# Performance work log

Measured on AMD Instinct MI355X. Metric: run time of the kernel, lower is better.

Reference implementation:

```python
import jax, jax.numpy as jnp
import numpy as np

HEADS = 8
DIM_HEAD = 64
DIM = 512
EPS = 1e-5


def setup_inputs() -> dict:
    key = jax.random.key(0)
    ks = jax.random.split(key, 4)
    b, n = 4, 2048
    inner = HEADS * DIM_HEAD
    x = jax.random.normal(ks[0], (b, n, DIM), dtype=jnp.float32)
    pose_bias = jax.random.normal(ks[1], (b, n), dtype=jnp.float32)
    ln_gamma = jnp.ones((DIM,), dtype=jnp.float32)
    ln_beta = jnp.zeros((DIM,), dtype=jnp.float32)
    w_qkv = jax.random.normal(ks[2], (DIM, 3 * inner), dtype=jnp.float32) * (DIM ** -0.5)
    w_out = jax.random.normal(ks[3], (inner, DIM), dtype=jnp.float32) * (inner ** -0.5)
    beta = jnp.float32(0.5)
    return {"x": x, "pose_bias": pose_bias, "ln_gamma": ln_gamma,
            "ln_beta": ln_beta, "w_qkv": w_qkv, "w_out": w_out, "beta": beta}


def reference(x, pose_bias, ln_gamma, ln_beta, w_qkv, w_out, beta):
    b, n, d = x.shape
    h, dh = HEADS, DIM_HEAD
    scale = dh ** -0.5
    # LayerNorm (biased variance, eps=1e-5, affine)
    mu = jnp.mean(x, axis=-1, keepdims=True)
    var = jnp.mean(jnp.square(x - mu), axis=-1, keepdims=True)
    xn = (x - mu) * jax.lax.rsqrt(var + EPS) * ln_gamma + ln_beta
    # fused QKV projection (no bias)
    qkv = xn @ w_qkv                                  # [b, n, 3*h*dh]
    q, k, v = jnp.split(qkv, 3, axis=-1)
    def to_heads(t):
        return t.reshape(b, n, h, dh).transpose(0, 2, 1, 3)  # [b, h, n, dh]
    q, k, v = to_heads(q), to_heads(k), to_heads(v)
    dots = jnp.einsum('bhnd,bhmd->bhnm', q, k) * scale  # [b, h, n, n]
    # additive pose bias: beta * (bias_i + bias_j), broadcast over heads
    pose_attn = beta * (pose_bias[:, None, :, None] + pose_bias[:, None, None, :])
    dots = dots + pose_attn
    attn = jax.nn.softmax(dots, axis=-1)
    out = jnp.einsum('bhnm,bhmd->bhnd', attn, v)       # [b, h, n, dh]
    out = out.transpose(0, 2, 1, 3).reshape(b, n, h * dh)
    return out @ w_out
```

## Files before the change

kernel.cpp:

```cpp
#include <hip/hip_runtime.h>

#define NH    8
#define DH    64
#define DIMD  512
#define NCTX  2048
#define NB    4
#define NROWS (NB * NCTX)
#define QKVN  (3 * DIMD)

typedef __attribute__((ext_vector_type(8))) short bf16x8;
typedef __attribute__((ext_vector_type(4))) float f32x4;

#define INV_LN2 1.44269504f
#define SCLOG   (0.125f * INV_LN2)

__device__ __forceinline__ unsigned short f2bits(float f) {
  unsigned u = __float_as_uint(f);
  u += 0x7fffu + ((u >> 16) & 1u);
  return (unsigned short)(u >> 16);
}
__device__ __forceinline__ float bits2f(unsigned short u) {
  return __uint_as_float(((unsigned)u) << 16);
}

__device__ __forceinline__ void gll16(const void* g, void* l) {
  __builtin_amdgcn_global_load_lds(
      (const __attribute__((address_space(1))) unsigned int*)g,
      (__attribute__((address_space(3))) unsigned int*)l, 16, 0, 0);
}
__device__ __forceinline__ void gll4(const void* g, void* l) {
  __builtin_amdgcn_global_load_lds(
      (const __attribute__((address_space(1))) unsigned int*)g,
      (__attribute__((address_space(3))) unsigned int*)l, 4, 0, 0);
}

__global__ __launch_bounds__(256) void lntc_kernel(
    const float* __restrict__ x,
    const float* __restrict__ gamma,
    const float* __restrict__ beta,
    unsigned short* __restrict__ xn,
    const float* __restrict__ in0, unsigned short* __restrict__ out0,
    const float* __restrict__ in1, unsigned short* __restrict__ out1) {
  __shared__ float T[64][65];
  if (blockIdx.x < 2048) {
    const int wid  = threadIdx.x >> 6;
    const int lane = threadIdx.x & 63;
    const int row  = blockIdx.x * 4 + wid;
    const float* xr = x + (size_t)row * DIMD + lane * 8;
    float v[8];
    const float4 a = *reinterpret_cast<const float4*>(xr);
    const float4 b = *reinterpret_cast<const float4*>(xr + 4);
    v[0] = a.x; v[1] = a.y; v[2] = a.z; v[3] = a.w;
    v[4] = b.x; v[5] = b.y; v[6] = b.z; v[7] = b.w;
    float s = 0.f;
#pragma unroll
    for (int i = 0; i < 8; ++i) s += v[i];
#pragma unroll
    for (int off = 32; off; off >>= 1) s += __shfl_down(s, off);
    s = __shfl(s, 0);
    const float mu = s * (1.f / DIMD);
    float ss = 0.f;
#pragma unroll
    for (int i = 0; i < 8; ++i) { float d = v[i] - mu; ss += d * d; }
#pragma unroll
    for (int off = 32; off; off >>= 1) ss += __shfl_down(ss, off);
    ss = __shfl(ss, 0);
    const float inv = rsqrtf(ss * (1.f / DIMD) + 1e-5f);
    const float4 g0 = *reinterpret_cast<const float4*>(gamma + lane * 8);
    const float4 g1 = *reinterpret_cast<const float4*>(gamma + lane * 8 + 4);
    const float4 b0 = *reinterpret_cast<const float4*>(beta + lane * 8);
    const float4 b1 = *reinterpret_cast<const float4*>(beta + lane * 8 + 4);
    float g[8] = {g0.x, g0.y, g0.z, g0.w, g1.x, g1.y, g1.z, g1.w};
    float be[8] = {b0.x, b0.y, b0.z, b0.w, b1.x, b1.y, b1.z, b1.w};
    bf16x8 o;
#pragma unroll
    for (int i = 0; i < 8; ++i)
      o[i] = (short)f2bits((v[i] - mu) * inv * g[i] + be[i]);
    *reinterpret_cast<bf16x8*>(xn + (size_t)row * DIMD + lane * 8) = o;
  } else {
    const int t = blockIdx.x - 2048;
    const int bx = t % 24, rest = t / 24;
    const int by = rest % 8, z = rest / 8;
    const int C = z ? DIMD : QKVN;
    if (z && bx >= DIMD / 64) return;
    const float* in = z ? in1 : in0;
    unsigned short* out = z ? out1 : out0;
    const int r0 = by * 64, c0 = bx * 64;
    const int ty = threadIdx.x >> 4, tx = threadIdx.x & 15;
#pragma unroll
    for (int i = 0; i < 4; ++i) {
      const int r = ty + i * 16;
      const float4 v = *reinterpret_cast<const float4*>(
          in + (size_t)(r0 + r) * C + c0 + tx * 4);
      T[r][tx * 4 + 0] = v.x; T[r][tx * 4 + 1] = v.y;
      T[r][tx * 4 + 2] = v.z; T[r][tx * 4 + 3] = v.w;
    }
    __syncthreads();
#pragma unroll
    for (int i = 0; i < 4; ++i) {
      const int c = ty + i * 16;
      ushort4 o;
      o.x = f2bits(T[tx * 4 + 0][c]); o.y = f2bits(T[tx * 4 + 1][c]);
      o.z = f2bits(T[tx * 4 + 2][c]); o.w = f2bits(T[tx * 4 + 3][c]);
      *reinterpret_cast<ushort4*>(out + (size_t)(c0 + c) * DIMD + r0 + tx * 4) = o;
    }
  }
}

__global__ __launch_bounds__(256) void vtrans_kernel(
    const unsigned short* __restrict__ qkv,
    const float* __restrict__ pb,
    const float* __restrict__ betap,
    unsigned short* __restrict__ cexp,
    unsigned short* __restrict__ vt) {
  __shared__ unsigned short T[64][68];
  const int jt = blockIdx.x, hi = blockIdx.y, bi = blockIdx.z;
  const int ty = threadIdx.x >> 4, tx = threadIdx.x & 15;
  const int j0 = jt * 64;
#pragma unroll
  for (int i = 0; i < 4; ++i) {
    const int j = ty + i * 16;
    const ushort4 v = *reinterpret_cast<const ushort4*>(
        qkv + (size_t)(bi * NCTX + j0 + j) * QKVN + 2 * DIMD + hi * DH + tx * 4);
    T[j][tx * 4 + 0] = v.x; T[j][tx * 4 + 1] = v.y;
    T[j][tx * 4 + 2] = v.z; T[j][tx * 4 + 3] = v.w;
  }
  const float bl2 = betap[0] * INV_LN2;
  const float4 pv = *reinterpret_cast<const float4*>(pb + bi * NCTX + j0 + tx * 4);
  ushort4 cb;
  cb.x = f2bits(exp2f(bl2 * pv.x)); cb.y = f2bits(exp2f(bl2 * pv.y));
  cb.z = f2bits(exp2f(bl2 * pv.z)); cb.w = f2bits(exp2f(bl2 * pv.w));
  if (hi == 0 && ty == 0)
    *reinterpret_cast<ushort4*>(cexp + bi * NCTX + j0 + tx * 4) = cb;
  const float c0 = bits2f(cb.x), c1 = bits2f(cb.y), c2 = bits2f(cb.z), c3 = bits2f(cb.w);
  __syncthreads();
#pragma unroll
  for (int i = 0; i < 4; ++i) {
    const int d = ty + i * 16;
    ushort4 o;
    o.x = f2bits(bits2f(T[tx * 4 + 0][d]) * c0);
    o.y = f2bits(bits2f(T[tx * 4 + 1][d]) * c1);
    o.z = f2bits(bits2f(T[tx * 4 + 2][d]) * c2);
    o.w = f2bits(bits2f(T[tx * 4 + 3][d]) * c3);
    *reinterpret_cast<ushort4*>(
        vt + ((size_t)(bi * NH + hi) * DH + d) * NCTX + j0 + tx * 4) = o;
  }
}

__device__ __forceinline__ void storeC(float* C, size_t idx, float v) { C[idx] = v; }
__device__ __forceinline__ void storeC(unsigned short* C, size_t idx, float v) { C[idx] = f2bits(v); }

template <typename CT, bool QS>
__global__ __launch_bounds__(256) void ggemm_kernel(
    const unsigned short* __restrict__ A, const unsigned short* __restrict__ Bt,
    CT* __restrict__ C, int M, int N, int K) {
  __shared__ __align__(16) unsigned short As[128 * 64];
  __shared__ __align__(16) unsigned short Bs[128 * 64];
  const int tid  = threadIdx.x;
  const int wave = tid >> 6, lane = tid & 63;
  const int quad = lane >> 4, l16 = lane & 15;
  const int wr = wave >> 1, wc = wave & 1;
  const int tm0 = blockIdx.y * 128, tn0 = blockIdx.x * 128;
  const int srow = wave * 8 + (lane >> 3);
  const int ssh  = (((lane & 7) * 16) ^ ((lane >> 3) << 4)) >> 1;
  const unsigned short* ap = A + (size_t)(tm0 + srow) * K + ssh;
  const unsigned short* bp = Bt + (size_t)(tn0 + srow) * K + ssh;
  const int xs = (l16 & 7) << 3;
  f32x4 acc[4][4];
#pragma unroll
  for (int i = 0; i < 4; ++i)
#pragma unroll
    for (int j = 0; j < 4; ++j) acc[i][j] = (f32x4){0.f, 0.f, 0.f, 0.f};

  for (int k0 = 0; k0 < K; k0 += 64) {
#pragma unroll
    for (int i = 0; i < 4; ++i) {
      gll16(ap + (size_t)(i * 32) * K + k0, &As[i * 2048 + wave * 512]);
      gll16(bp + (size_t)(i * 32) * K + k0, &Bs[i * 2048 + wave * 512]);
    }
    __syncthreads();
#pragma unroll
    for (int kc = 0; kc < 2; ++kc) {
      const int kk = ((kc * 32 + quad * 8) ^ xs);
      bf16x8 af[4], bfr[4];
#pragma unroll
      for (int i = 0; i < 4; ++i)
        af[i] = *reinterpret_cast<const bf16x8*>(&As[(wr * 64 + i * 16 + l16) * 64 + kk]);
#pragma unroll
      for (int j = 0; j < 4; ++j)
        bfr[j] = *reinterpret_cast<const bf16x8*>(&Bs[(wc * 64 + j * 16 + l16) * 64 + kk]);
#pragma unroll
      for (int i = 0; i < 4; ++i)
#pragma unroll
        for (int j = 0; j < 4; ++j)
          acc[i][j] = __builtin_amdgcn_mfma_f32_16x16x32_bf16(af[i], bfr[j], acc[i][j], 0, 0, 0);
    }
    __syncthreads();
  }
#pragma unroll
  for (int j = 0; j < 4; ++j) {
    const int col = tn0 + wc * 64 + j * 16 + l16;
    const float scl = (QS && col < DIMD) ? SCLOG : 1.0f;
#pragma unroll
    for (int i = 0; i < 4; ++i)
#pragma unroll
      for (int r = 0; r < 4; ++r)
        storeC(C, (size_t)(tm0 + wr * 64 + i * 16 + quad * 4 + r) * N + col,
               acc[i][j][r] * scl);
  }
}

template <typename CT, bool QS>
__global__ __launch_bounds__(256) void mgemm_kernel(
    const unsigned short* __restrict__ A, const unsigned short* __restrict__ Bt,
    CT* __restrict__ C, int M, int N, int K) {
  __shared__ __align__(16) unsigned short As[128][72];
  __shared__ __align__(16) unsigned short Bs[128][72];
  const int tid  = threadIdx.x;
  const int wave = tid >> 6, lane = tid & 63;
  const int quad = lane >> 4, l16 = lane & 15;
  const int wr = wave >> 1, wc = wave & 1;
  const int tm0 = blockIdx.y * 128, tn0 = blockIdx.x * 128;
  const int srow = tid >> 3;
  const int schunk = (tid & 7) * 8;
  f32x4 acc[4][4];
#pragma unroll
  for (int i = 0; i < 4; ++i)
#pragma unroll
    for (int j = 0; j < 4; ++j) acc[i][j] = (f32x4){0.f, 0.f, 0.f, 0.f};

  bf16x8 ra[4], rb[4];
#pragma unroll
  for (int p = 0; p < 4; ++p) {
    const int r = srow + p * 32;
    ra[p] = *reinterpret_cast<const bf16x8*>(A + (size_t)(tm0 + r) * K + schunk);
    rb[p] = *reinterpret_cast<const bf16x8*>(Bt + (size_t)(tn0 + r) * K + schunk);
  }
  for (int k0 = 0; k0 < K; k0 += 64) {
#pragma unroll
    for (int p = 0; p < 4; ++p) {
      const int r = srow + p * 32;
      *reinterpret_cast<bf16x8*>(&As[r][schunk]) = ra[p];
      *reinterpret_cast<bf16x8*>(&Bs[r][schunk]) = rb[p];
    }
    __syncthreads();
    if (k0 + 64 < K) {
#pragma unroll
      for (int p = 0; p < 4; ++p) {
        const int r = srow + p * 32;
        ra[p] = *reinterpret_cast<const bf16x8*>(A + (size_t)(tm0 + r) * K + k0 + 64 + schunk);
        rb[p] = *reinterpret_cast<const bf16x8*>(Bt + (size_t)(tn0 + r) * K + k0 + 64 + schunk);
      }
    }
#pragma unroll
    for (int kc = 0; kc < 2; ++kc) {
      const int kk = kc * 32 + quad * 8;
      bf16x8 af[4], bfr[4];
#pragma unroll
      for (int i = 0; i < 4; ++i)
        af[i] = *reinterpret_cast<const bf16x8*>(&As[wr * 64 + i * 16 + l16][kk]);
#pragma unroll
      for (int j = 0; j < 4; ++j)
        bfr[j] = *reinterpret_cast<const bf16x8*>(&Bs[wc * 64 + j * 16 + l16][kk]);
#pragma unroll
      for (int i = 0; i < 4; ++i)
#pragma unroll
        for (int j = 0; j < 4; ++j)
          acc[i][j] = __builtin_amdgcn_mfma_f32_16x16x32_bf16(af[i], bfr[j], acc[i][j], 0, 0, 0);
    }
    __syncthreads();
  }
#pragma unroll
  for (int j = 0; j < 4; ++j) {
    const int col = tn0 + wc * 64 + j * 16 + l16;
    const float scl = (QS && col < DIMD) ? SCLOG : 1.0f;
#pragma unroll
    for (int i = 0; i < 4; ++i)
#pragma unroll
      for (int r = 0; r < 4; ++r)
        storeC(C, (size_t)(tm0 + wr * 64 + i * 16 + quad * 4 + r) * N + col,
               acc[i][j][r] * scl);
  }
}

__global__ __launch_bounds__(256, 4) void fattn_kernel(
    const unsigned short* __restrict__ qkv,
    const unsigned short* __restrict__ vtg,
    const unsigned short* __restrict__ cexp,
    unsigned short* __restrict__ out) {
  __shared__ __align__(16) unsigned short lds[2][8320];

  const int qt = blockIdx.x, hi = blockIdx.y, bi = blockIdx.z;
  const int tid  = threadIdx.x;
  const int wave = tid >> 6, lane = tid & 63;
  const int quad = lane >> 4, l16 = lane & 15;
  const int wq = wave & 1, wk = wave >> 1;
  const int qrow0 = qt * 64;
  const unsigned short* base  = qkv + (size_t)bi * NCTX * QKVN + hi * DH;
  const unsigned short* vbase = vtg + (size_t)(bi * NH + hi) * DH * NCTX;
  const unsigned short* cbase = cexp + (size_t)bi * NCTX;

  const int sr8 = lane >> 3;
  const int ssh = ((((lane & 7) * 16) ^ (sr8 << 4)) >> 1);
  const unsigned short* kp0 = base + (size_t)(wave * 8 + sr8) * QKVN + DIMD + ssh;
  const unsigned short* kp1 = kp0 + (size_t)32 * QKVN;
  const unsigned short* vp0 = vbase + (size_t)(wave * 8 + sr8) * NCTX + ssh;
  const unsigned short* vp1 = vp0 + (size_t)32 * NCTX;
  const unsigned short* cp  = cbase + (tid & 31) * 2;

#define STAGE(buf)                                    \
  gll16(kp0, &(buf)[wave * 512]);                     \
  gll16(kp1, &(buf)[2048 + wave * 512]);              \
  gll16(vp0, &(buf)[4096 + wave * 512]);              \
  gll16(vp1, &(buf)[6144 + wave * 512]);              \
  if (tid < 32) gll4(cp, &(buf)[8192]);               \
  kp0 += (size_t)64 * QKVN; kp1 += (size_t)64 * QKVN; \
  vp0 += 64; vp1 += 64; cp += 64;

  bf16x8 qf[2][2];
#pragma unroll
  for (int u = 0; u < 2; ++u)
#pragma unroll
    for (int h = 0; h < 2; ++h)
      qf[u][h] = *reinterpret_cast<const bf16x8*>(
          base + (size_t)(qrow0 + wq * 32 + u * 16 + l16) * QKVN + h * 32 + quad * 8);

  const int xs = (l16 & 7) << 3;
  const int kofs0 = (wk * 32 + l16) * 64 + ((quad * 8) ^ xs);
  const int kofs1 = (wk * 32 + l16) * 64 + ((32 + quad * 8) ^ xs);
  const int vofs  = 4096 + l16 * 64 + ((wk * 32 + quad * 8) ^ xs);
  const int cofs  = 8192 + wk * 32 + quad * 8;

  STAGE(lds[0]);
  __syncthreads();

  f32x4 O[2][4], accl[2];
#pragma unroll
  for (int u = 0; u < 2; ++u) {
    accl[u] = (f32x4){0.f, 0.f, 0.f, 0.f};
#pragma unroll
    for (int s = 0; s < 4; ++s) O[u][s] = (f32x4){0.f, 0.f, 0.f, 0.f};
  }

  for (int kt = 0; kt < 32; ++kt) {
    const unsigned short* bc = lds[kt & 1];
    if (kt < 31) { STAGE(lds[(kt & 1) ^ 1]); }
    f32x4 sfr[2][2];
#pragma unroll
    for (int t = 0; t < 2; ++t) {
      const bf16x8 kf0 = *reinterpret_cast<const bf16x8*>(&bc[kofs0 + t * 1024]);
      const bf16x8 kf1 = *reinterpret_cast<const bf16x8*>(&bc[kofs1 + t * 1024]);
#pragma unroll
      for (int u = 0; u < 2; ++u) {
        f32x4 acc = (f32x4){0.f, 0.f, 0.f, 0.f};
        acc = __builtin_amdgcn_mfma_f32_16x16x32_bf16(kf0, qf[u][0], acc, 0, 0, 0);
        acc = __builtin_amdgcn_mfma_f32_16x16x32_bf16(kf1, qf[u][1], acc, 0, 0, 0);
        sfr[t][u] = acc;
      }
    }
    bf16x8 pf[2];
#pragma unroll
    for (int u = 0; u < 2; ++u) {
      const unsigned a0 = __float_as_uint(__builtin_amdgcn_exp2f(sfr[0][u][0])) + 0x8000u;
      const unsigned a1 = __float_as_uint(__builtin_amdgcn_exp2f(sfr[0][u][1])) + 0x8000u;
      const unsigned a2 = __float_as_uint(__builtin_amdgcn_exp2f(sfr[0][u][2])) + 0x8000u;
      const unsigned a3 = __float_as_uint(__builtin_amdgcn_exp2f(sfr[0][u][3])) + 0x8000u;
      const unsigned b0 = __float_as_uint(__builtin_amdgcn_exp2f(sfr[1][u][0])) + 0x8000u;
      const unsigned b1 = __float_as_uint(__builtin_amdgcn_exp2f(sfr[1][u][1])) + 0x8000u;
      const unsigned b2 = __float_as_uint(__builtin_amdgcn_exp2f(sfr[1][u][2])) + 0x8000u;
      const unsigned b3 = __float_as_uint(__builtin_amdgcn_exp2f(sfr[1][u][3])) + 0x8000u;
      unsigned x0 = __builtin_amdgcn_perm(a1, a0, 0x07060302u);
      unsigned x1 = __builtin_amdgcn_perm(a3, a2, 0x07060302u);
      unsigned y0 = __builtin_amdgcn_perm(b1, b0, 0x07060302u);
      unsigned y1 = __builtin_amdgcn_perm(b3, b2, 0x07060302u);
      asm("v_permlane32_swap_b32 %0, %1" : "+v"(x0), "+v"(y0));
      asm("v_permlane32_swap_b32 %0, %1" : "+v"(x1), "+v"(y1));
      asm("v_permlane16_swap_b32 %0, %1" : "+v"(x0), "+v"(y0));
      asm("v_permlane16_swap_b32 %0, %1" : "+v"(x1), "+v"(y1));
      union { unsigned q[4]; bf16x8 v; } pu;
      pu.q[0] = x0; pu.q[1] = x1; pu.q[2] = y0; pu.q[3] = y1;
      pf[u] = pu.v;
    }
    {
      const bf16x8 cf = *reinterpret_cast<const bf16x8*>(&bc[cofs]);
      accl[0] = __builtin_amdgcn_mfma_f32_16x16x32_bf16(pf[0], cf, accl[0], 0, 0, 0);
      accl[1] = __builtin_amdgcn_mfma_f32_16x16x32_bf16(pf[1], cf, accl[1], 0, 0, 0);
#pragma unroll
      for (int s = 0; s < 4; ++s) {
        const bf16x8 bv = *reinterpret_cast<const bf16x8*>(&bc[vofs + s * 1024]);
        O[0][s] = __builtin_amdgcn_mfma_f32_16x16x32_bf16(pf[0], bv, O[0][s], 0, 0, 0);
        O[1][s] = __builtin_amdgcn_mfma_f32_16x16x32_bf16(pf[1], bv, O[1][s], 0, 0, 0);
      }
    }
    __syncthreads();
  }
#undef STAGE
  unsigned short* Ob = (unsigned short*)lds;
  float* lb = (float*)((unsigned short*)lds + 4352);
  if (wk == 1) {
#pragma unroll
    for (int u = 0; u < 2; ++u) {
#pragma unroll
      for (int s = 0; s < 4; ++s)
#pragma unroll
        for (int r = 0; r < 4; ++r)
          Ob[(wq * 32 + u * 16 + quad * 4 + r) * 68 + s * 16 + l16] = f2bits(O[u][s][r]);
      if (l16 == 0)
#pragma unroll
        for (int r = 0; r < 4; ++r)
          lb[64 + wq * 32 + u * 16 + quad * 4 + r] = accl[u][r];
    }
  } else {
#pragma unroll
    for (int u = 0; u < 2; ++u)
      if (l16 == 0)
#pragma unroll
        for (int r = 0; r < 4; ++r)
          lb[wq * 32 + u * 16 + quad * 4 + r] = accl[u][r];
  }
  __syncthreads();
  if (wk == 0) {
#pragma unroll
    for (int u = 0; u < 2; ++u)
#pragma unroll
      for (int r = 0; r < 4; ++r) {
        const int ql = wq * 32 + u * 16 + quad * 4 + r;
        const float linv = 1.f / (lb[ql] + lb[64 + ql]);
        const size_t orow = ((size_t)bi * NCTX + qrow0 + ql) * DIMD + hi * DH;
#pragma unroll
        for (int s = 0; s < 4; ++s)
          out[orow + s * 16 + l16] =
              f2bits((O[u][s][r] + bits2f(Ob[ql * 68 + s * 16 + l16])) * linv);
      }
  }
}

extern "C" void kernel_launch(void* const* d_in, const int* in_sizes, int n_in,
                              void* d_out, int out_size, void* d_ws, size_t ws_size,
                              hipStream_t stream) {
  const float* x     = (const float*)d_in[0];
  const float* pose  = (const float*)d_in[1];
  const float* gam   = (const float*)d_in[2];
  const float* bet   = (const float*)d_in[3];
  const float* wqkv  = (const float*)d_in[4];
  const float* wout  = (const float*)d_in[5];
  const float* betap = (const float*)d_in[6];
  float* out = (float*)d_out;

  unsigned short* xn    = (unsigned short*)d_ws;
  unsigned short* qkvb  = xn + (size_t)NROWS * DIMD;
  unsigned short* wqkvT = qkvb + (size_t)NROWS * QKVN;
  unsigned short* woutT = wqkvT + (size_t)QKVN * DIMD;
  unsigned short* vtg   = woutT + (size_t)DIMD * DIMD;
  unsigned short* cexp  = vtg + (size_t)NB * NH * DH * NCTX;
  unsigned short* aout  = xn;

  lntc_kernel<<<2048 + 384, 256, 0, stream>>>(
      x, gam, bet, xn, wqkv, wqkvT, wout, woutT);
  ggemm_kernel<unsigned short, true><<<dim3(QKVN / 128, NROWS / 128), 256, 0, stream>>>(
      xn, wqkvT, qkvb, NROWS, QKVN, DIMD);
  vtrans_kernel<<<dim3(NCTX / 64, NH, NB), 256, 0, stream>>>(
      qkvb, pose, betap, cexp, vtg);
  fattn_kernel<<<dim3(NCTX / 64, NH, NB), 256, 0, stream>>>(qkvb, vtg, cexp, aout);
  mgemm_kernel<float, false><<<dim3(DIMD / 128, NROWS / 128), 256, 0, stream>>>(
      aout, woutT, out, NROWS, DIMD, DIMD);
}
```

Before: 168.1 us.

## Fuse V transpose into QKV GEMM epilogue and add pose bias inside score MFMA

Removes the separate vtrans kernel. The QKV GEMM now computes V tiles with swapped MFMA operands and writes transposed V directly into the head-major layout. The key-side pose bias is precomputed as beta/ln2 times pose in fp32 by extra blocks in the LN kernel, then loaded into LDS and used as the MFMA accumulator initial value for the scores. Because the bias is no longer folded into V and the row sums as exp weights, the row-sum MFMA uses a constant ones vector. The gains are one fewer launch and one fewer pass over V, paid for with scattered 2-byte stores in the GEMM epilogue and a larger fp32 bias stage in attention.

```diff
diff --git a/kernel.cpp b/kernel.cpp
--- a/kernel.cpp
+++ b/kernel.cpp
@@ -40,7 +40,9 @@
     const float* __restrict__ beta,
     unsigned short* __restrict__ xn,
     const float* __restrict__ in0, unsigned short* __restrict__ out0,
-    const float* __restrict__ in1, unsigned short* __restrict__ out1) {
+    const float* __restrict__ in1, unsigned short* __restrict__ out1,
+    const float* __restrict__ pb, const float* __restrict__ betap,
+    float* __restrict__ pbl) {
   __shared__ float T[64][65];
   if (blockIdx.x < 2048) {
     const int wid  = threadIdx.x >> 6;
@@ -77,7 +79,7 @@
     for (int i = 0; i < 8; ++i)
       o[i] = (short)f2bits((v[i] - mu) * inv * g[i] + be[i]);
     *reinterpret_cast<bf16x8*>(xn + (size_t)row * DIMD + lane * 8) = o;
-  } else {
+  } else if (blockIdx.x < 2432) {
     const int t = blockIdx.x - 2048;
     const int bx = t % 24, rest = t / 24;
     const int by = rest % 8, z = rest / 8;
@@ -104,46 +106,16 @@
       o.z = f2bits(T[tx * 4 + 2][c]); o.w = f2bits(T[tx * 4 + 3][c]);
       *reinterpret_cast<ushort4*>(out + (size_t)(c0 + c) * DIMD + r0 + tx * 4) = o;
     }
-  }
-}
-
-__global__ __launch_bounds__(256) void vtrans_kernel(
-    const unsigned short* __restrict__ qkv,
-    const float* __restrict__ pb,
-    const float* __restrict__ betap,
-    unsigned short* __restrict__ cexp,
-    unsigned short* __restrict__ vt) {
-  __shared__ unsigned short T[64][68];
-  const int jt = blockIdx.x, hi = blockIdx.y, bi = blockIdx.z;
-  const int ty = threadIdx.x >> 4, tx = threadIdx.x & 15;
-  const int j0 = jt * 64;
-#pragma unroll
-  for (int i = 0; i < 4; ++i) {
-    const int j = ty + i * 16;
-    const ushort4 v = *reinterpret_cast<const ushort4*>(
-        qkv + (size_t)(bi * NCTX + j0 + j) * QKVN + 2 * DIMD + hi * DH + tx * 4);
-    T[j][tx * 4 + 0] = v.x; T[j][tx * 4 + 1] = v.y;
-    T[j][tx * 4 + 2] = v.z; T[j][tx * 4 + 3] = v.w;
-  }
-  const float bl2 = betap[0] * INV_LN2;
-  const float4 pv = *reinterpret_cast<const float4*>(pb + bi * NCTX + j0 + tx * 4);
-  ushort4 cb;
-  cb.x = f2bits(exp2f(bl2 * pv.x)); cb.y = f2bits(exp2f(bl2 * pv.y));
-  cb.z = f2bits(exp2f(bl2 * pv.z)); cb.w = f2bits(exp2f(bl2 * pv.w));
-  if (hi == 0 && ty == 0)
-    *reinterpret_cast<ushort4*>(cexp + bi * NCTX + j0 + tx * 4) = cb;
-  const float c0 = bits2f(cb.x), c1 = bits2f(cb.y), c2 = bits2f(cb.z), c3 = bits2f(cb.w);
-  __syncthreads();
-#pragma unroll
-  for (int i = 0; i < 4; ++i) {
-    const int d = ty + i * 16;
-    ushort4 o;
-    o.x = f2bits(bits2f(T[tx * 4 + 0][d]) * c0);
-    o.y = f2bits(bits2f(T[tx * 4 + 1][d]) * c1);
-    o.z = f2bits(bits2f(T[tx * 4 + 2][d]) * c2);
-    o.w = f2bits(bits2f(T[tx * 4 + 3][d]) * c3);
-    *reinterpret_cast<ushort4*>(
-        vt + ((size_t)(bi * NH + hi) * DH + d) * NCTX + j0 + tx * 4) = o;
+  } else {
+    const int t2 = blockIdx.x - 2432;
+    const float bl2 = betap[0] * INV_LN2;
+    const int idx = t2 * 2048 + threadIdx.x * 8;
+    const float4 a = *reinterpret_cast<const float4*>(pb + idx);
+    const float4 b = *reinterpret_cast<const float4*>(pb + idx + 4);
+    float4 oa = {bl2 * a.x, bl2 * a.y, bl2 * a.z, bl2 * a.w};
+    float4 ob = {bl2 * b.x, bl2 * b.y, bl2 * b.z, bl2 * b.w};
+    *reinterpret_cast<float4*>(pbl + idx) = oa;
+    *reinterpret_cast<float4*>(pbl + idx + 4) = ob;
   }
 }
 
@@ -153,7 +125,7 @@
 template <typename CT, bool QS>
 __global__ __launch_bounds__(256) void ggemm_kernel(
     const unsigned short* __restrict__ A, const unsigned short* __restrict__ Bt,
-    CT* __restrict__ C, int M, int N, int K) {
+    CT* __restrict__ C, unsigned short* __restrict__ vtg, int M, int N, int K) {
   __shared__ __align__(16) unsigned short As[128 * 64];
   __shared__ __align__(16) unsigned short Bs[128 * 64];
   const int tid  = threadIdx.x;
@@ -161,6 +133,7 @@
   const int quad = lane >> 4, l16 = lane & 15;
   const int wr = wave >> 1, wc = wave & 1;
   const int tm0 = blockIdx.y * 128, tn0 = blockIdx.x * 128;
+  const bool vswap = QS && (tn0 >= 2 * DIMD);
   const int srow = wave * 8 + (lane >> 3);
   const int ssh  = (((lane & 7) * 16) ^ ((lane >> 3) << 4)) >> 1;
   const unsigned short* ap = A + (size_t)(tm0 + srow) * K + ssh;
@@ -189,24 +162,47 @@
 #pragma unroll
       for (int j = 0; j < 4; ++j)
         bfr[j] = *reinterpret_cast<const bf16x8*>(&Bs[(wc * 64 + j * 16 + l16) * 64 + kk]);
+      if (vswap) {
+#pragma unroll
+        for (int i = 0; i < 4; ++i)
+#pragma unroll
+          for (int j = 0; j < 4; ++j)
+            acc[i][j] = __builtin_amdgcn_mfma_f32_16x16x32_bf16(bfr[j], af[i], acc[i][j], 0, 0, 0);
+      } else {
+#pragma unroll
+        for (int i = 0; i < 4; ++i)
+#pragma unroll
+          for (int j = 0; j < 4; ++j)
+            acc[i][j] = __builtin_amdgcn_mfma_f32_16x16x32_bf16(af[i], bfr[j], acc[i][j], 0, 0, 0);
+      }
+    }
+    __syncthreads();
+  }
+  if (vswap) {
+#pragma unroll
+    for (int j = 0; j < 4; ++j)
 #pragma unroll
       for (int i = 0; i < 4; ++i)
 #pragma unroll
-        for (int j = 0; j < 4; ++j)
-          acc[i][j] = __builtin_amdgcn_mfma_f32_16x16x32_bf16(af[i], bfr[j], acc[i][j], 0, 0, 0);
-    }
-    __syncthreads();
-  }
-#pragma unroll
-  for (int j = 0; j < 4; ++j) {
-    const int col = tn0 + wc * 64 + j * 16 + l16;
-    const float scl = (QS && col < DIMD) ? SCLOG : 1.0f;
-#pragma unroll
-    for (int i = 0; i < 4; ++i)
-#pragma unroll
-      for (int r = 0; r < 4; ++r)
-        storeC(C, (size_t)(tm0 + wr * 64 + i * 16 + quad * 4 + r) * N + col,
-               acc[i][j][r] * scl);
+        for (int r = 0; r < 4; ++r) {
+          const int vcol = tn0 - 2 * DIMD + wc * 64 + j * 16 + quad * 4 + r;
+          const int hi = vcol >> 6, d = vcol & 63;
+          const int rowc = tm0 + wr * 64 + i * 16 + l16;
+          const int bi = rowc >> 11, jc = rowc & (NCTX - 1);
+          vtg[((size_t)(bi * NH + hi) * DH + d) * NCTX + jc] = f2bits(acc[i][j][r]);
+        }
+  } else {
+#pragma unroll
+    for (int j = 0; j < 4; ++j) {
+      const int col = tn0 + wc * 64 + j * 16 + l16;
+      const float scl = (QS && col < DIMD) ? SCLOG : 1.0f;
+#pragma unroll
+      for (int i = 0; i < 4; ++i)
+#pragma unroll
+        for (int r = 0; r < 4; ++r)
+          storeC(C, (size_t)(tm0 + wr * 64 + i * 16 + quad * 4 + r) * N + col,
+                 acc[i][j][r] * scl);
+    }
   }
 }
 
@@ -286,7 +282,7 @@
 __global__ __launch_bounds__(256, 4) void fattn_kernel(
     const unsigned short* __restrict__ qkv,
     const unsigned short* __restrict__ vtg,
-    const unsigned short* __restrict__ cexp,
+    const float* __restrict__ pbl,
     unsigned short* __restrict__ out) {
   __shared__ __align__(16) unsigned short lds[2][8320];
 
@@ -298,7 +294,7 @@
   const int qrow0 = qt * 64;
   const unsigned short* base  = qkv + (size_t)bi * NCTX * QKVN + hi * DH;
   const unsigned short* vbase = vtg + (size_t)(bi * NH + hi) * DH * NCTX;
-  const unsigned short* cbase = cexp + (size_t)bi * NCTX;
+  const float* pbase = pbl + (size_t)bi * NCTX;
 
   const int sr8 = lane >> 3;
   const int ssh = ((((lane & 7) * 16) ^ (sr8 << 4)) >> 1);
@@ -306,16 +302,16 @@
   const unsigned short* kp1 = kp0 + (size_t)32 * QKVN;
   const unsigned short* vp0 = vbase + (size_t)(wave * 8 + sr8) * NCTX + ssh;
   const unsigned short* vp1 = vp0 + (size_t)32 * NCTX;
-  const unsigned short* cp  = cbase + (tid & 31) * 2;
+  const float* pp = pbase + lane;
 
 #define STAGE(buf)                                    \
   gll16(kp0, &(buf)[wave * 512]);                     \
   gll16(kp1, &(buf)[2048 + wave * 512]);              \
   gll16(vp0, &(buf)[4096 + wave * 512]);              \
   gll16(vp1, &(buf)[6144 + wave * 512]);              \
-  if (tid < 32) gll4(cp, &(buf)[8192]);               \
+  if (tid < 64) gll4(pp, &(buf)[8192]);               \
   kp0 += (size_t)64 * QKVN; kp1 += (size_t)64 * QKVN; \
-  vp0 += 64; vp1 += 64; cp += 64;
+  vp0 += 64; vp1 += 64; pp += 64;
 
   bf16x8 qf[2][2];
 #pragma unroll
@@ -329,7 +325,9 @@
   const int kofs0 = (wk * 32 + l16) * 64 + ((quad * 8) ^ xs);
   const int kofs1 = (wk * 32 + l16) * 64 + ((32 + quad * 8) ^ xs);
   const int vofs  = 4096 + l16 * 64 + ((wk * 32 + quad * 8) ^ xs);
-  const int cofs  = 8192 + wk * 32 + quad * 8;
+  const int pofs  = wk * 32 + quad * 4;
+
+  const bf16x8 ones = {16256, 16256, 16256, 16256, 16256, 16256, 16256, 16256};
 
   STAGE(lds[0]);
   __syncthreads();
@@ -345,14 +343,16 @@
   for (int kt = 0; kt < 32; ++kt) {
     const unsigned short* bc = lds[kt & 1];
     if (kt < 31) { STAGE(lds[(kt & 1) ^ 1]); }
+    const float* pblf = (const float*)(bc + 8192);
     f32x4 sfr[2][2];
 #pragma unroll
     for (int t = 0; t < 2; ++t) {
       const bf16x8 kf0 = *reinterpret_cast<const bf16x8*>(&bc[kofs0 + t * 1024]);
       const bf16x8 kf1 = *reinterpret_cast<const bf16x8*>(&bc[kofs1 + t * 1024]);
+      const f32x4 bias = *reinterpret_cast<const f32x4*>(&pblf[pofs + t * 16]);
 #pragma unroll
       for (int u = 0; u < 2; ++u) {
-        f32x4 acc = (f32x4){0.f, 0.f, 0.f, 0.f};
+        f32x4 acc = bias;
         acc = __builtin_amdgcn_mfma_f32_16x16x32_bf16(kf0, qf[u][0], acc, 0, 0, 0);
         acc = __builtin_amdgcn_mfma_f32_16x16x32_bf16(kf1, qf[u][1], acc, 0, 0, 0);
         sfr[t][u] = acc;
@@ -382,9 +382,8 @@
       pf[u] = pu.v;
     }
     {
-      const bf16x8 cf = *reinterpret_cast<const bf16x8*>(&bc[cofs]);
-      accl[0] = __builtin_amdgcn_mfma_f32_16x16x32_bf16(pf[0], cf, accl[0], 0, 0, 0);
-      accl[1] = __builtin_amdgcn_mfma_f32_16x16x32_bf16(pf[1], cf, accl[1], 0, 0, 0);
+      accl[0] = __builtin_amdgcn_mfma_f32_16x16x32_bf16(pf[0], ones, accl[0], 0, 0, 0);
+      accl[1] = __builtin_amdgcn_mfma_f32_16x16x32_bf16(pf[1], ones, accl[1], 0, 0, 0);
 #pragma unroll
       for (int s = 0; s < 4; ++s) {
         const bf16x8 bv = *reinterpret_cast<const bf16x8*>(&bc[vofs + s * 1024]);
@@ -452,16 +451,14 @@
   unsigned short* wqkvT = qkvb + (size_t)NROWS * QKVN;
   unsigned short* woutT = wqkvT + (size_t)QKVN * DIMD;
   unsigned short* vtg   = woutT + (size_t)DIMD * DIMD;
-  unsigned short* cexp  = vtg + (size_t)NB * NH * DH * NCTX;
+  float*          pbl   = (float*)(vtg + (size_t)NB * NH * DH * NCTX);
   unsigned short* aout  = xn;
 
-  lntc_kernel<<<2048 + 384, 256, 0, stream>>>(
-      x, gam, bet, xn, wqkv, wqkvT, wout, woutT);
+  lntc_kernel<<<2048 + 384 + 4, 256, 0, stream>>>(
+      x, gam, bet, xn, wqkv, wqkvT, wout, woutT, pose, betap, pbl);
   ggemm_kernel<unsigned short, true><<<dim3(QKVN / 128, NROWS / 128), 256, 0, stream>>>(
-      xn, wqkvT, qkvb, NROWS, QKVN, DIMD);
-  vtrans_kernel<<<dim3(NCTX / 64, NH, NB), 256, 0, stream>>>(
-      qkvb, pose, betap, cexp, vtg);
-  fattn_kernel<<<dim3(NCTX / 64, NH, NB), 256, 0, stream>>>(qkvb, vtg, cexp, aout);
+      xn, wqkvT, qkvb, vtg, NROWS, QKVN, DIMD);
+  fattn_kernel<<<dim3(NCTX / 64, NH, NB), 256, 0, stream>>>(qkvb, vtg, pbl, aout);
   mgemm_kernel<float, false><<<dim3(DIMD / 128, NROWS / 128), 256, 0, stream>>>(
       aout, woutT, out, NROWS, DIMD, DIMD);
 }
```

Measured after the change: 166.3 us. Within noise of the previous version (-1.1%).
